# Performance work log

Measured on AMD Instinct MI355X. Metric: run time of the kernel, lower is better.

## Reference

```python
import jax, jax.numpy as jnp
import numpy as np

C_IN, LAT, OUT, EMB = 3, 64, 512, 5
B, H = 128, 128
KS = [4, 4, 3, 4, 2]                       # per-layer dynamic kernel sizes
CHANS = [C_IN, LAT, LAT * 2, LAT * 4, LAT * 8]  # in-channels of each dyn conv
MIX = [(C_IN, LAT), (LAT, LAT * 2), (LAT * 2, LAT * 4), (LAT * 4, LAT * 8), (LAT * 8, OUT)]


def setup_inputs() -> dict:
    key = jax.random.key(0)
    ks = jax.random.split(key, 40)
    nrm = lambda k, shape, s=0.02: jax.random.normal(k, shape, jnp.float32) * s
    inp = {}
    inp["input"] = jax.random.normal(ks[0], (B, C_IN, H, H), jnp.float32)
    inp["label"] = jax.random.randint(ks[1], (B,), 0, 10)
    inp["emb"] = nrm(ks[2], (10, EMB), 1.0)  # label embedding table
    i = 3
    for j, (c, k) in enumerate(zip(CHANS, KS), 1):  # label -> dyn kernel linears
        inp[f"l{j}_w"] = nrm(ks[i], (EMB, c * k * k), 0.1)
        inp[f"l{j}_b"] = jnp.zeros((c * k * k,), jnp.float32)
        i += 1
    for j, (ci, co) in enumerate(MIX, 1):  # channel-mixer linears
        inp[f"cm{j}_w"] = nrm(ks[i], (ci, co))
        inp[f"cm{j}_b"] = jnp.zeros((co,), jnp.float32)
        i += 1
    for j, c in enumerate([LAT, LAT * 2, LAT * 4, LAT * 8], 1):  # BN affine params
        inp[f"bn{j}_g"] = jnp.ones((c,), jnp.float32)
        inp[f"bn{j}_b"] = jnp.zeros((c,), jnp.float32)
    return inp


def dw_conv(x, k, stride, pad):
    """Per-sample, per-channel (depthwise) 2d cross-correlation.
    x: (B,C,H,W), k: (B,C,h,w) -> (B,C,H',W')."""
    def one(xi, ki):
        return jax.lax.conv_general_dilated(
            xi[None], ki[:, None], (stride, stride),
            [(pad, pad), (pad, pad)],
            dimension_numbers=("NCHW", "OIHW", "NCHW"),
            feature_group_count=xi.shape[0])[0]
    return jax.vmap(one)(x, k)


def reference(input, label, emb,
              l1_w, l1_b, l2_w, l2_b, l3_w, l3_b, l4_w, l4_b, l5_w, l5_b,
              cm1_w, cm1_b, cm2_w, cm2_b, cm3_w, cm3_b, cm4_w, cm4_b, cm5_w, cm5_b,
              bn1_g, bn1_b, bn2_g, bn2_b, bn3_g, bn3_b, bn4_g, bn4_b):
    e = emb[label]  # (B, EMB)
    dk = lambda w, b, c, k: jnp.tanh(e @ w + b).reshape(-1, c, k, k)
    k1 = dk(l1_w, l1_b, C_IN, 4)
    k2 = dk(l2_w, l2_b, LAT, 4)
    k3 = dk(l3_w, l3_b, LAT * 2, 3)
    k4 = dk(l4_w, l4_b, LAT * 4, 4)
    k5 = dk(l5_w, l5_b, LAT * 8, 2)

    mix = lambda z, w, b: jnp.einsum("bchw,cd->bdhw", z, w) + b[None, :, None, None]
    lrelu = lambda z: jax.nn.leaky_relu(z, 0.2)

    def bn(z, g, b):  # training-mode BN (batch statistics, biased var, eps=1e-5)
        m = z.mean((0, 2, 3), keepdims=True)
        v = z.var((0, 2, 3), keepdims=True)
        return (z - m) * jax.lax.rsqrt(v + 1e-5) * g[None, :, None, None] + b[None, :, None, None]

    z = bn(lrelu(mix(dw_conv(input, k1, 2, 1), cm1_w, cm1_b)), bn1_g, bn1_b)
    z = bn(lrelu(mix(dw_conv(z, k2, 2, 1), cm2_w, cm2_b)), bn2_g, bn2_b)
    z = bn(lrelu(mix(dw_conv(z, k3, 2, 1), cm3_w, cm3_b)), bn3_g, bn3_b)
    z = bn(lrelu(mix(dw_conv(z, k4, 2, 1), cm4_w, cm4_b)), bn4_g, bn4_b)
    z = jax.nn.sigmoid(mix(dw_conv(z, k5, 1, 0), cm5_w, cm5_b))  # (B, OUT, 7, 7)
    return (z, label)
```

## Files before the change

kernel.cpp:

```cpp
#include <hip/hip_runtime.h>
#include <hip/hip_bf16.h>

typedef __hip_bfloat16 bf16;
using short8  = __attribute__((ext_vector_type(8))) short;
using floatx4 = __attribute__((ext_vector_type(4))) float;

__device__ __forceinline__ float b2f(unsigned short u) {
    union { unsigned int i; float f; } v; v.i = ((unsigned int)u) << 16; return v.f;
}
__device__ __forceinline__ unsigned short f2b(float f) {
    bf16 h = __float2bfloat16(f);
    return *(unsigned short*)&h;
}

#define NREP 16

__global__ __launch_bounds__(256) void prep_kernel(
    const int* __restrict__ label, const float* __restrict__ emb,
    const float* __restrict__ l1w, const float* __restrict__ l1b,
    const float* __restrict__ l2w, const float* __restrict__ l2b,
    const float* __restrict__ l3w, const float* __restrict__ l3b,
    const float* __restrict__ l4w, const float* __restrict__ l4b,
    const float* __restrict__ l5w, const float* __restrict__ l5b,
    float* __restrict__ dynk, float* __restrict__ stats,
    float* __restrict__ labelOut)
{
    const int tid = threadIdx.x;
    if (blockIdx.x == gridDim.x - 1) {
        for (int i = tid; i < 30720; i += 256) stats[i] = 0.0f;
        if (tid < 128) labelOut[tid] = (float)label[tid];
        return;
    }
    int idx = blockIdx.x * 256 + tid;
    if (idx >= 1071104) return;
    const float* w; const float* bb; int loc, ckk;
    if (idx < 6144)        { w = l1w; bb = l1b; loc = idx;          ckk = 48;   }
    else if (idx < 137216) { w = l2w; bb = l2b; loc = idx - 6144;   ckk = 1024; }
    else if (idx < 284672) { w = l3w; bb = l3b; loc = idx - 137216; ckk = 1152; }
    else if (idx < 808960) { w = l4w; bb = l4b; loc = idx - 284672; ckk = 4096; }
    else                   { w = l5w; bb = l5b; loc = idx - 808960; ckk = 2048; }
    int b   = loc / ckk;
    int col = loc - b * ckk;
    int lab = label[b];
    float acc = bb[col];
    #pragma unroll
    for (int m = 0; m < 5; ++m)
        acc = fmaf(emb[lab * 5 + m], w[m * ckk + col], acc);
    dynk[idx] = tanhf(acc);
}

__global__ __launch_bounds__(256) void wt_kernel(
    const float* __restrict__ w2, const float* __restrict__ w3,
    const float* __restrict__ w4, const float* __restrict__ w5,
    bf16* __restrict__ wt2, bf16* __restrict__ wt3,
    bf16* __restrict__ wt4, bf16* __restrict__ wt5)
{
    __shared__ float T[32][33];
    const int tid = threadIdx.x;
    int t = blockIdx.x;
    const float* W; bf16* WT; int K, N, tl;
    if (t < 8)        { W = w2; WT = wt2; K = 64;  N = 128; tl = t; }
    else if (t < 40)  { W = w3; WT = wt3; K = 128; N = 256; tl = t - 8; }
    else if (t < 168) { W = w4; WT = wt4; K = 256; N = 512; tl = t - 40; }
    else              { W = w5; WT = wt5; K = 512; N = 512; tl = t - 168; }
    const int NT = N >> 5;
    const int kt = tl / NT, nt = tl - kt * NT;
    const int k0 = kt * 32, n0 = nt * 32;
    const int cc = tid & 31, rr = tid >> 5;
    #pragma unroll
    for (int it = 0; it < 4; ++it) {
        int k = rr + it * 8;
        T[k][cc] = W[(long)(k0 + k) * N + n0 + cc];
    }
    __syncthreads();
    #pragma unroll
    for (int it = 0; it < 4; ++it) {
        int n = rr + it * 8;
        WT[(long)(n0 + n) * K + k0 + cc] = __float2bfloat16(T[cc][n]);
    }
}

__global__ __launch_bounds__(128) void fused_l1_v3(
    const float* __restrict__ xf, const float* __restrict__ dynk,
    const float* __restrict__ W, const float* __restrict__ bias,
    bf16* __restrict__ y, float* __restrict__ statsOut)
{
    constexpr int HIN = 128, HOUT = 64;
    constexpr int TW = 16, TH = 8;
    constexpr int PS  = 36;
    constexpr int PCH = 18 * PS;

    __shared__ float patch[3 * PCH];
    __shared__ __align__(16) float dwT[16 * 28];
    __shared__ float Wlds[192];
    __shared__ float klds[48];
    __shared__ float biasL[64];
    __shared__ float sums[64], sqs[64];

    const int tid = threadIdx.x;
    const int b   = blockIdx.x >> 5;
    const int tl  = blockIdx.x & 31;
    const int ty0 = (tl >> 2) * TH;
    const int tx0 = (tl & 3) * TW;

    if (tid < 48) klds[tid] = dynk[b * 48 + tid];
    for (int i = tid; i < 192; i += 128) Wlds[i] = W[i];
    if (tid < 64) { biasL[tid] = bias[tid]; sums[tid] = 0.f; sqs[tid] = 0.f; }

    {
        const int iy0 = ty0 * 2 - 1, ix0 = tx0 * 2 - 1;
        for (int i = tid; i < 3 * 18 * 34; i += 128) {
            int c  = i / 612;
            int r  = i - c * 612;
            int py = r / 34, px = r - py * 34;
            int gy = iy0 + py, gx = ix0 + px;
            float v = 0.f;
            if ((unsigned)gy < (unsigned)HIN && (unsigned)gx < (unsigned)HIN)
                v = xf[((long)b * 3 + c) * (HIN * HIN) + gy * HIN + gx];
            patch[c * PCH + py * PS + px] = v;
        }
    }
    __syncthreads();

    {
        const int py = tid >> 4, px = tid & 15;
        const int pixg = tid >> 3, j = tid & 7;
        #pragma unroll
        for (int c = 0; c < 3; ++c) {
            const float* pb = &patch[c * PCH + (py * 2) * PS + px * 2];
            float a = 0.f;
            #pragma unroll
            for (int kh = 0; kh < 4; ++kh)
                #pragma unroll
                for (int kw = 0; kw < 4; ++kw)
                    a = fmaf(pb[kh * PS + kw], klds[c * 16 + kh * 4 + kw], a);
            dwT[pixg * 28 + j * 3 + c] = a;
        }
    }
    __syncthreads();

    {
        const int cq = tid & 7, pixg = tid >> 3;
        const int d0 = cq * 8;
        float Wr[3][8], bi[8];
        #pragma unroll
        for (int c = 0; c < 3; ++c)
            #pragma unroll
            for (int t = 0; t < 8; ++t) Wr[c][t] = Wlds[c * 64 + d0 + t];
        #pragma unroll
        for (int t = 0; t < 8; ++t) bi[t] = biasL[d0 + t];

        float dv[24];
        #pragma unroll
        for (int q4 = 0; q4 < 6; ++q4)
            *(float4*)&dv[q4 * 4] = *(const float4*)&dwT[pixg * 28 + q4 * 4];

        float sreg[8] = {}, qreg[8] = {};
        #pragma unroll
        for (int j = 0; j < 8; ++j) {
            const int pos = pixg * 8 + j;
            const float dv0 = dv[j * 3 + 0];
            const float dv1 = dv[j * 3 + 1];
            const float dv2 = dv[j * 3 + 2];
            const int py = pos >> 4, px = pos & 15;
            const long row = ((long)(b * HOUT + ty0 + py)) * HOUT + tx0 + px;
            union { uint4 v; unsigned short us[8]; } pk;
            #pragma unroll
            for (int t = 0; t < 8; ++t) {
                float v = fmaf(dv0, Wr[0][t], fmaf(dv1, Wr[1][t], fmaf(dv2, Wr[2][t], bi[t])));
                v = v > 0.f ? v : 0.2f * v;
                sreg[t] += v;
                qreg[t] = fmaf(v, v, qreg[t]);
                pk.us[t] = f2b(v);
            }
            *(uint4*)&y[row * 64 + d0] = pk.v;
        }
        #pragma unroll
        for (int m = 8; m < 64; m <<= 1)
            #pragma unroll
            for (int t = 0; t < 8; ++t) {
                sreg[t] += __shfl_xor(sreg[t], m);
                qreg[t] += __shfl_xor(qreg[t], m);
            }
        if ((tid & 63) < 8) {
            #pragma unroll
            for (int t = 0; t < 8; ++t) {
                atomicAdd(&sums[d0 + t], sreg[t]);
                atomicAdd(&sqs [d0 + t], qreg[t]);
            }
        }
    }
    __syncthreads();
    {
        const int rep = blockIdx.x & (NREP - 1);
        if (tid < 64) {
            atomicAdd(&statsOut[rep * 128 + tid],      sums[tid]);
            atomicAdd(&statsOut[rep * 128 + 64 + tid], sqs[tid]);
        }
    }
}

template<int C, int KS, int HIN, int HOUT, int STRIDE, int PAD, int NTHR>
__global__ __launch_bounds__(NTHR) void dw_direct(
    const bf16* __restrict__ x, const float* __restrict__ st,
    const float* __restrict__ gam, const float* __restrict__ bet,
    const float* __restrict__ dynk, bf16* __restrict__ outA, float NINV)
{
    constexpr int G   = C / 8;
    constexpr int KSK = KS * KS;
    static_assert(NTHR == HOUT * G, "one output row per block");

    __shared__ float wlds[KSK * C];
    __shared__ float ksumL[C];
    __shared__ float scaleL[C], shiftL[C];

    const int tid = threadIdx.x;
    const int b   = blockIdx.x / HOUT;
    const int oy  = blockIdx.x % HOUT;

    for (int i = tid; i < KSK * C; i += NTHR) {
        int c = i % C, t = i / C;
        wlds[t * C + c] = dynk[((long)b * C + c) * KSK + t];
    }
    for (int c = tid; c < C; c += NTHR) {
        float s = 0.f, q = 0.f;
        #pragma unroll
        for (int r = 0; r < NREP; ++r) {
            s += st[r * 2 * C + c];
            q += st[r * 2 * C + C + c];
        }
        float m   = s * NINV;
        float var = fmaf(q, NINV, -m * m);
        float scv = gam[c] * rsqrtf(var + 1e-5f);
        scaleL[c] = scv;
        shiftL[c] = fmaf(-m, scv, bet[c]);
    }
    __syncthreads();
    for (int c = tid; c < C; c += NTHR) {
        float s = 0.f;
        #pragma unroll
        for (int t = 0; t < KSK; ++t) s += wlds[t * C + c];
        ksumL[c] = s;
    }
    __syncthreads();

    const int g  = tid % G;
    const int ox = tid / G;
    const int c0 = g * 8;
    const int iy0 = oy * STRIDE - PAD;
    const int ix0 = ox * STRIDE - PAD;

    float acc[8];
    #pragma unroll
    for (int ch = 0; ch < 8; ++ch) acc[ch] = 0.f;

    const bool interior = (iy0 >= 0) && (iy0 + KS <= HIN) &&
                          (ix0 >= 0) && (ix0 + KS <= HIN);
    float r[8];

    if (interior) {
        const bf16* bp = x + ((long)(b * HIN + iy0) * HIN + ix0) * C + c0;
        uint4 v[KSK];
        #pragma unroll
        for (int kh = 0; kh < KS; ++kh)
            #pragma unroll
            for (int kw = 0; kw < KS; ++kw)
                v[kh * KS + kw] = *(const uint4*)(bp + (kh * HIN + kw) * C);
        #pragma unroll
        for (int t = 0; t < KSK; ++t) {
            const float* wp = &wlds[t * C + c0];
            float4 wa = *(const float4*)wp;
            float4 wb = *(const float4*)(wp + 4);
            const float wt[8] = {wa.x, wa.y, wa.z, wa.w, wb.x, wb.y, wb.z, wb.w};
            #pragma unroll
            for (int ch = 0; ch < 8; ++ch) {
                unsigned u = ((const unsigned*)&v[t])[ch >> 1];
                unsigned bits = (ch & 1) ? (u & 0xffff0000u) : (u << 16);
                acc[ch] = fmaf(__uint_as_float(bits), wt[ch], acc[ch]);
            }
        }
        #pragma unroll
        for (int ch = 0; ch < 8; ++ch) {
            float sc = scaleL[c0 + ch], sh = shiftL[c0 + ch], ks = ksumL[c0 + ch];
            r[ch] = fmaf(sc, acc[ch], sh * ks);
        }
    } else {
        float sc[8], sh[8];
        #pragma unroll
        for (int ch = 0; ch < 8; ++ch) { sc[ch] = scaleL[c0 + ch]; sh[ch] = shiftL[c0 + ch]; }
        #pragma unroll
        for (int kh = 0; kh < KS; ++kh) {
            const int iy = iy0 + kh;
            if ((unsigned)iy >= (unsigned)HIN) continue;
            #pragma unroll
            for (int kw = 0; kw < KS; ++kw) {
                const int ix = ix0 + kw;
                if ((unsigned)ix >= (unsigned)HIN) continue;
                uint4 v = *(const uint4*)&x[((long)(b * HIN + iy) * HIN + ix) * C + c0];
                const float* wp = &wlds[(kh * KS + kw) * C + c0];
                float4 wa = *(const float4*)wp;
                float4 wb = *(const float4*)(wp + 4);
                const float wt[8] = {wa.x, wa.y, wa.z, wa.w, wb.x, wb.y, wb.z, wb.w};
                #pragma unroll
                for (int ch = 0; ch < 8; ++ch) {
                    unsigned u = ((const unsigned*)&v)[ch >> 1];
                    unsigned bits = (ch & 1) ? (u & 0xffff0000u) : (u << 16);
                    float xb = fmaf(__uint_as_float(bits), sc[ch], sh[ch]);
                    acc[ch] = fmaf(xb, wt[ch], acc[ch]);
                }
            }
        }
        #pragma unroll
        for (int ch = 0; ch < 8; ++ch) r[ch] = acc[ch];
    }

    union { uint4 v; unsigned short us[8]; } pk;
    #pragma unroll
    for (int ch = 0; ch < 8; ++ch) pk.us[ch] = f2b(r[ch]);
    *(uint4*)&outA[((long)(b * HOUT + oy) * HOUT + ox) * C + c0] = pk.v;
}

template<int K, int COUT, bool LAST>
__global__ __launch_bounds__(256) void gemm_layer(
    const bf16* __restrict__ A, const bf16* __restrict__ WT,
    const float* __restrict__ bias, bf16* __restrict__ y,
    float* __restrict__ statsOut, float* __restrict__ outF, int Mtiles)
{
    constexpr int SK = 72;
    constexpr int CS = 136;
    __shared__ __align__(16) unsigned short smem[18432];
    unsigned short* As  = smem;
    unsigned short* Bs  = smem + 9216;
    unsigned short* Csh = smem;
    __shared__ float sums[128], sqs[128];

    const int tid  = threadIdx.x;
    const int lane = tid & 63;
    const int w    = tid >> 6;
    const int wm   = (w >> 1) * 64, wn = (w & 1) * 64;
    const int lm   = lane & 15, lq = lane >> 4;
    const int mt   = blockIdx.x % Mtiles;
    const int nt   = blockIdx.x / Mtiles;
    const long m0  = (long)mt * 128;
    const int  n0  = nt * 128;

    floatx4 acc[4][4];
    #pragma unroll
    for (int i = 0; i < 4; ++i)
        #pragma unroll
        for (int j = 0; j < 4; ++j) acc[i][j] = (floatx4)0.0f;

    for (int kb = 0; kb < K; kb += 64) {
        __syncthreads();
        #pragma unroll
        for (int s = 0; s < 4; ++s) {
            int i = tid + s * 256;
            int m = i >> 3, q = i & 7;
            uint4 va = *(const uint4*)(A  + ((m0 + m) * K + kb + q * 8));
            uint4 vb = *(const uint4*)(WT + ((long)(n0 + m) * K + kb + q * 8));
            *(uint4*)&As[m * SK + q * 8] = va;
            *(uint4*)&Bs[m * SK + q * 8] = vb;
        }
        __syncthreads();
        #pragma unroll
        for (int h = 0; h < 2; ++h) {
            short8 af[4], bfr[4];
            #pragma unroll
            for (int i = 0; i < 4; ++i) {
                af[i]  = *(const short8*)&As[(wm + i * 16 + lm) * SK + h * 32 + lq * 8];
                bfr[i] = *(const short8*)&Bs[(wn + i * 16 + lm) * SK + h * 32 + lq * 8];
            }
            #pragma unroll
            for (int i = 0; i < 4; ++i)
                #pragma unroll
                for (int j = 0; j < 4; ++j)
                    acc[i][j] = __builtin_amdgcn_mfma_f32_16x16x32_bf16(af[i], bfr[j], acc[i][j], 0, 0, 0);
        }
    }
    __syncthreads();

    float bj[4];
    #pragma unroll
    for (int j = 0; j < 4; ++j) bj[j] = bias[n0 + wn + j * 16 + lm];

    if constexpr (!LAST) {
        if (tid < 128) { sums[tid] = 0.f; sqs[tid] = 0.f; }
        #pragma unroll
        for (int i = 0; i < 4; ++i)
            #pragma unroll
            for (int j = 0; j < 4; ++j) {
                int c = wn + j * 16 + lm;
                #pragma unroll
                for (int rg = 0; rg < 4; ++rg) {
                    int r = wm + i * 16 + lq * 4 + rg;
                    float v = acc[i][j][rg] + bj[j];
                    v = v > 0.f ? v : 0.2f * v;
                    Csh[r * CS + c] = f2b(v);
                }
            }
        __syncthreads();
        const int cg = tid & 15, mr = tid >> 4;
        float sacc[8], qacc[8];
        #pragma unroll
        for (int t = 0; t < 8; ++t) { sacc[t] = 0.f; qacc[t] = 0.f; }
        #pragma unroll
        for (int it = 0; it < 8; ++it) {
            int m = mr + it * 16;
            uint4 pk = *(const uint4*)&Csh[m * CS + cg * 8];
            *(uint4*)&y[(m0 + m) * COUT + n0 + cg * 8] = pk;
            const unsigned short* pu = (const unsigned short*)&pk;
            #pragma unroll
            for (int t = 0; t < 8; ++t) {
                float f = b2f(pu[t]);
                sacc[t] += f;
                qacc[t] = fmaf(f, f, qacc[t]);
            }
        }
        #pragma unroll
        for (int t = 0; t < 8; ++t) {
            atomicAdd(&sums[cg * 8 + t], sacc[t]);
            atomicAdd(&sqs [cg * 8 + t], qacc[t]);
        }
        __syncthreads();
        {
            const int rep = blockIdx.x & (NREP - 1);
            if (tid < 128) {
                atomicAdd(&statsOut[rep * 2 * COUT + n0 + tid],        sums[tid]);
                atomicAdd(&statsOut[rep * 2 * COUT + COUT + n0 + tid], sqs[tid]);
            }
        }
    } else {
        #pragma unroll
        for (int i = 0; i < 4; ++i)
            #pragma unroll
            for (int j = 0; j < 4; ++j) {
                int c  = wn + j * 16 + lm;
                int rb = wm + i * 16 + lq * 4;
                ushort4 pk;
                unsigned short* pp = (unsigned short*)&pk;
                #pragma unroll
                for (int rg = 0; rg < 4; ++rg)
                    pp[rg] = f2b(acc[i][j][rg] + bj[j]);
                *(ushort4*)&Csh[c * CS + rb] = pk;
            }
        __syncthreads();
        const int mg = tid & 15, nr = tid >> 4;
        #pragma unroll
        for (int it = 0; it < 8; ++it) {
            int n = nr + it * 16;
            uint4 pk = *(const uint4*)&Csh[n * CS + mg * 8];
            const unsigned short* pu = (const unsigned short*)&pk;
            #pragma unroll
            for (int t = 0; t < 8; ++t) {
                int m = (int)m0 + mg * 8 + t;
                int b = m / 49, pos = m - b * 49;
                float v = b2f(pu[t]);
                outF[((long)(b * 512 + n0 + n)) * 49 + pos] = 1.f / (1.f + __expf(-v));
            }
        }
    }
}


extern "C" void kernel_launch(void* const* d_in, const int* in_sizes, int n_in,
                              void* d_out, int out_size, void* d_ws, size_t ws_size,
                              hipStream_t stream)
{
    const float* input = (const float*)d_in[0];
    const int*   label = (const int*)d_in[1];
    const float* emb   = (const float*)d_in[2];
    const float* lw[5] = {(const float*)d_in[3], (const float*)d_in[5], (const float*)d_in[7],
                          (const float*)d_in[9], (const float*)d_in[11]};
    const float* lb[5] = {(const float*)d_in[4], (const float*)d_in[6], (const float*)d_in[8],
                          (const float*)d_in[10], (const float*)d_in[12]};
    const float* cmw[5] = {(const float*)d_in[13], (const float*)d_in[15], (const float*)d_in[17],
                           (const float*)d_in[19], (const float*)d_in[21]};
    const float* cmb[5] = {(const float*)d_in[14], (const float*)d_in[16], (const float*)d_in[18],
                           (const float*)d_in[20], (const float*)d_in[22]};
    const float* bng[4] = {(const float*)d_in[23], (const float*)d_in[25],
                           (const float*)d_in[27], (const float*)d_in[29]};
    const float* bnb[4] = {(const float*)d_in[24], (const float*)d_in[26],
                           (const float*)d_in[28], (const float*)d_in[30]};
    float* out = (float*)d_out;

    float* wsf   = (float*)d_ws;
    float* dynk  = wsf;
    float* stats = wsf + 1071104;
    const float* k1 = dynk;
    const float* k2 = dynk + 6144;
    const float* k3 = dynk + 137216;
    const float* k4 = dynk + 284672;
    const float* k5 = dynk + 808960;
    float* st1 = stats;
    float* st2 = stats + 2048;
    float* st3 = stats + 6144;
    float* st4 = stats + 14336;

    bf16* wt  = (bf16*)((char*)d_ws + 4407296);
    bf16* wt2 = wt;
    bf16* wt3 = wt + 8192;
    bf16* wt4 = wt + 40960;
    bf16* wt5 = wt + 172032;
    bf16* S1  = (bf16*)((char*)d_ws + 5308416);
    bf16* S2  = (bf16*)((char*)d_ws + 72417280);

    prep_kernel<<<4186, 256, 0, stream>>>(label, emb,
        lw[0], lb[0], lw[1], lb[1], lw[2], lb[2], lw[3], lb[3], lw[4], lb[4],
        dynk, stats, out + 3211264);
    wt_kernel<<<424, 256, 0, stream>>>(cmw[1], cmw[2], cmw[3], cmw[4],
                                       wt2, wt3, wt4, wt5);

    fused_l1_v3<<<4096, 128, 0, stream>>>(input, k1, cmw[0], cmb[0], S1, st1);

    dw_direct<64, 4, 64, 32, 2, 1, 256><<<4096, 256, 0, stream>>>(
        S1, st1, bng[0], bnb[0], k2, S2, 1.f / 524288.f);
    gemm_layer<64, 128, false><<<1024, 256, 0, stream>>>(
        S2, wt2, cmb[1], S1, st2, nullptr, 1024);

    dw_direct<128, 3, 32, 16, 2, 1, 256><<<2048, 256, 0, stream>>>(
        S1, st2, bng[1], bnb[1], k3, S2, 1.f / 131072.f);
    gemm_layer<128, 256, false><<<512, 256, 0, stream>>>(
        S2, wt3, cmb[2], S1, st3, nullptr, 256);

    dw_direct<256, 4, 16, 8, 2, 1, 256><<<1024, 256, 0, stream>>>(
        S1, st3, bng[2], bnb[2], k4, S2, 1.f / 32768.f);
    gemm_layer<256, 512, false><<<256, 256, 0, stream>>>(
        S2, wt4, cmb[3], S1, st4, nullptr, 64);

    dw_direct<512, 2, 8, 7, 1, 0, 448><<<896, 448, 0, stream>>>(
        S1, st4, bng[3], bnb[3], k5, S2, 1.f / 8192.f);
    gemm_layer<512, 512, true><<<196, 256, 0, stream>>>(
        S2, wt5, cmb[4], nullptr, nullptr, out, 49);
}
```

Measured before the change: 347.8 us.

## Pretranspose dynamic kernels and hoist BN affine prep out of depthwise conv

The prep kernel now writes the dynamic depthwise kernels in a tap-major (t, c) layout, so each dw_direct block copies its weights to shared memory with contiguous float4 loads instead of a strided gather. BN scale and shift are computed once per layer by a small bn_prep kernel rather than redundantly in every block. The interior path applies the affine to each input before the multiply, which removes the ksum precompute and one barrier. The cost is four extra kernel launches and more FMAs per tap in the inner loop.

```diff
diff --git a/kernel.cpp b/kernel.cpp
--- a/kernel.cpp
+++ b/kernel.cpp
@@ -33,12 +33,12 @@
     }
     int idx = blockIdx.x * 256 + tid;
     if (idx >= 1071104) return;
-    const float* w; const float* bb; int loc, ckk;
-    if (idx < 6144)        { w = l1w; bb = l1b; loc = idx;          ckk = 48;   }
-    else if (idx < 137216) { w = l2w; bb = l2b; loc = idx - 6144;   ckk = 1024; }
-    else if (idx < 284672) { w = l3w; bb = l3b; loc = idx - 137216; ckk = 1152; }
-    else if (idx < 808960) { w = l4w; bb = l4b; loc = idx - 284672; ckk = 4096; }
-    else                   { w = l5w; bb = l5b; loc = idx - 808960; ckk = 2048; }
+    const float* w; const float* bb; int loc, ckk, ksk, base;
+    if (idx < 6144)        { w = l1w; bb = l1b; loc = idx;          ckk = 48;   ksk = 0;  base = 0;      }
+    else if (idx < 137216) { w = l2w; bb = l2b; loc = idx - 6144;   ckk = 1024; ksk = 16; base = 6144;   }
+    else if (idx < 284672) { w = l3w; bb = l3b; loc = idx - 137216; ckk = 1152; ksk = 9;  base = 137216; }
+    else if (idx < 808960) { w = l4w; bb = l4b; loc = idx - 284672; ckk = 4096; ksk = 16; base = 284672; }
+    else                   { w = l5w; bb = l5b; loc = idx - 808960; ckk = 2048; ksk = 4;  base = 808960; }
     int b   = loc / ckk;
     int col = loc - b * ckk;
     int lab = label[b];
@@ -46,7 +46,34 @@
     #pragma unroll
     for (int m = 0; m < 5; ++m)
         acc = fmaf(emb[lab * 5 + m], w[m * ckk + col], acc);
-    dynk[idx] = tanhf(acc);
+    float val = tanhf(acc);
+    if (ksk == 0) {
+        dynk[idx] = val;
+    } else {
+        int c  = col / ksk;
+        int t  = col - c * ksk;
+        int Cl = ckk / ksk;
+        dynk[base + b * ckk + t * Cl + c] = val;
+    }
+}
+
+__global__ void bn_prep(const float* __restrict__ st,
+                        const float* __restrict__ gam, const float* __restrict__ bet,
+                        float* __restrict__ aff, int C, float NINV)
+{
+    int c = threadIdx.x;
+    if (c >= C) return;
+    float s = 0.f, q = 0.f;
+    #pragma unroll
+    for (int r = 0; r < NREP; ++r) {
+        s += st[r * 2 * C + c];
+        q += st[r * 2 * C + C + c];
+    }
+    float m   = s * NINV;
+    float var = fmaf(q, NINV, -m * m);
+    float sc  = gam[c] * rsqrtf(var + 1e-5f);
+    aff[c]     = sc;
+    aff[C + c] = fmaf(-m, sc, bet[c]);
 }
 
 __global__ __launch_bounds__(256) void wt_kernel(
@@ -202,45 +229,23 @@
 
 template<int C, int KS, int HIN, int HOUT, int STRIDE, int PAD, int NTHR>
 __global__ __launch_bounds__(NTHR) void dw_direct(
-    const bf16* __restrict__ x, const float* __restrict__ st,
-    const float* __restrict__ gam, const float* __restrict__ bet,
-    const float* __restrict__ dynk, bf16* __restrict__ outA, float NINV)
+    const bf16* __restrict__ x, const float* __restrict__ aff,
+    const float* __restrict__ dynkT, bf16* __restrict__ outA)
 {
     constexpr int G   = C / 8;
     constexpr int KSK = KS * KS;
     static_assert(NTHR == HOUT * G, "one output row per block");
 
-    __shared__ float wlds[KSK * C];
-    __shared__ float ksumL[C];
-    __shared__ float scaleL[C], shiftL[C];
+    __shared__ __align__(16) float wlds[KSK * C];
 
     const int tid = threadIdx.x;
     const int b   = blockIdx.x / HOUT;
     const int oy  = blockIdx.x % HOUT;
 
-    for (int i = tid; i < KSK * C; i += NTHR) {
-        int c = i % C, t = i / C;
-        wlds[t * C + c] = dynk[((long)b * C + c) * KSK + t];
-    }
-    for (int c = tid; c < C; c += NTHR) {
-        float s = 0.f, q = 0.f;
-        #pragma unroll
-        for (int r = 0; r < NREP; ++r) {
-            s += st[r * 2 * C + c];
-            q += st[r * 2 * C + C + c];
-        }
-        float m   = s * NINV;
-        float var = fmaf(q, NINV, -m * m);
-        float scv = gam[c] * rsqrtf(var + 1e-5f);
-        scaleL[c] = scv;
-        shiftL[c] = fmaf(-m, scv, bet[c]);
-    }
-    __syncthreads();
-    for (int c = tid; c < C; c += NTHR) {
-        float s = 0.f;
-        #pragma unroll
-        for (int t = 0; t < KSK; ++t) s += wlds[t * C + c];
-        ksumL[c] = s;
+    {
+        const float* src = dynkT + (long)b * (KSK * C);
+        for (int i = tid * 4; i < KSK * C; i += NTHR * 4)
+            *(float4*)&wlds[i] = *(const float4*)&src[i];
     }
     __syncthreads();
 
@@ -250,13 +255,24 @@
     const int iy0 = oy * STRIDE - PAD;
     const int ix0 = ox * STRIDE - PAD;
 
+    float sc[8], sh[8];
+    {
+        float4 a0 = *(const float4*)&aff[c0];
+        float4 a1 = *(const float4*)&aff[c0 + 4];
+        float4 b0 = *(const float4*)&aff[C + c0];
+        float4 b1 = *(const float4*)&aff[C + c0 + 4];
+        sc[0]=a0.x; sc[1]=a0.y; sc[2]=a0.z; sc[3]=a0.w;
+        sc[4]=a1.x; sc[5]=a1.y; sc[6]=a1.z; sc[7]=a1.w;
+        sh[0]=b0.x; sh[1]=b0.y; sh[2]=b0.z; sh[3]=b0.w;
+        sh[4]=b1.x; sh[5]=b1.y; sh[6]=b1.z; sh[7]=b1.w;
+    }
+
     float acc[8];
     #pragma unroll
     for (int ch = 0; ch < 8; ++ch) acc[ch] = 0.f;
 
     const bool interior = (iy0 >= 0) && (iy0 + KS <= HIN) &&
                           (ix0 >= 0) && (ix0 + KS <= HIN);
-    float r[8];
 
     if (interior) {
         const bf16* bp = x + ((long)(b * HIN + iy0) * HIN + ix0) * C + c0;
@@ -276,18 +292,11 @@
             for (int ch = 0; ch < 8; ++ch) {
                 unsigned u = ((const unsigned*)&v[t])[ch >> 1];
                 unsigned bits = (ch & 1) ? (u & 0xffff0000u) : (u << 16);
-                acc[ch] = fmaf(__uint_as_float(bits), wt[ch], acc[ch]);
-            }
-        }
-        #pragma unroll
-        for (int ch = 0; ch < 8; ++ch) {
-            float sc = scaleL[c0 + ch], sh = shiftL[c0 + ch], ks = ksumL[c0 + ch];
-            r[ch] = fmaf(sc, acc[ch], sh * ks);
+                float xb = fmaf(__uint_as_float(bits), sc[ch], sh[ch]);
+                acc[ch] = fmaf(xb, wt[ch], acc[ch]);
+            }
         }
     } else {
-        float sc[8], sh[8];
-        #pragma unroll
-        for (int ch = 0; ch < 8; ++ch) { sc[ch] = scaleL[c0 + ch]; sh[ch] = shiftL[c0 + ch]; }
         #pragma unroll
         for (int kh = 0; kh < KS; ++kh) {
             const int iy = iy0 + kh;
@@ -310,13 +319,11 @@
                 }
             }
         }
-        #pragma unroll
-        for (int ch = 0; ch < 8; ++ch) r[ch] = acc[ch];
     }
 
     union { uint4 v; unsigned short us[8]; } pk;
     #pragma unroll
-    for (int ch = 0; ch < 8; ++ch) pk.us[ch] = f2b(r[ch]);
+    for (int ch = 0; ch < 8; ++ch) pk.us[ch] = f2b(acc[ch]);
     *(uint4*)&outA[((long)(b * HOUT + oy) * HOUT + ox) * C + c0] = pk.v;
 }
 
@@ -486,11 +493,11 @@
     float* wsf   = (float*)d_ws;
     float* dynk  = wsf;
     float* stats = wsf + 1071104;
-    const float* k1 = dynk;
-    const float* k2 = dynk + 6144;
-    const float* k3 = dynk + 137216;
-    const float* k4 = dynk + 284672;
-    const float* k5 = dynk + 808960;
+    const float* k1  = dynk;
+    const float* k2T = dynk + 6144;
+    const float* k3T = dynk + 137216;
+    const float* k4T = dynk + 284672;
+    const float* k5T = dynk + 808960;
     float* st1 = stats;
     float* st2 = stats + 2048;
     float* st3 = stats + 6144;
@@ -503,6 +510,11 @@
     bf16* wt5 = wt + 172032;
     bf16* S1  = (bf16*)((char*)d_ws + 5308416);
     bf16* S2  = (bf16*)((char*)d_ws + 72417280);
+    float* affBase = (float*)((char*)d_ws + 89194496);
+    float* aff1 = affBase;
+    float* aff2 = affBase + 128;
+    float* aff3 = affBase + 384;
+    float* aff4 = affBase + 896;
 
     prep_kernel<<<4186, 256, 0, stream>>>(label, emb,
         lw[0], lb[0], lw[1], lb[1], lw[2], lb[2], lw[3], lb[3], lw[4], lb[4],
@@ -512,23 +524,23 @@
 
     fused_l1_v3<<<4096, 128, 0, stream>>>(input, k1, cmw[0], cmb[0], S1, st1);
 
-    dw_direct<64, 4, 64, 32, 2, 1, 256><<<4096, 256, 0, stream>>>(
-        S1, st1, bng[0], bnb[0], k2, S2, 1.f / 524288.f);
+    bn_prep<<<1, 64, 0, stream>>>(st1, bng[0], bnb[0], aff1, 64, 1.f / 524288.f);
+    dw_direct<64, 4, 64, 32, 2, 1, 256><<<4096, 256, 0, stream>>>(S1, aff1, k2T, S2);
     gemm_layer<64, 128, false><<<1024, 256, 0, stream>>>(
         S2, wt2, cmb[1], S1, st2, nullptr, 1024);
 
-    dw_direct<128, 3, 32, 16, 2, 1, 256><<<2048, 256, 0, stream>>>(
-        S1, st2, bng[1], bnb[1], k3, S2, 1.f / 131072.f);
+    bn_prep<<<1, 128, 0, stream>>>(st2, bng[1], bnb[1], aff2, 128, 1.f / 131072.f);
+    dw_direct<128, 3, 32, 16, 2, 1, 256><<<2048, 256, 0, stream>>>(S1, aff2, k3T, S2);
     gemm_layer<128, 256, false><<<512, 256, 0, stream>>>(
         S2, wt3, cmb[2], S1, st3, nullptr, 256);
 
-    dw_direct<256, 4, 16, 8, 2, 1, 256><<<1024, 256, 0, stream>>>(
-        S1, st3, bng[2], bnb[2], k4, S2, 1.f / 32768.f);
+    bn_prep<<<1, 256, 0, stream>>>(st3, bng[2], bnb[2], aff3, 256, 1.f / 32768.f);
+    dw_direct<256, 4, 16, 8, 2, 1, 256><<<1024, 256, 0, stream>>>(S1, aff3, k4T, S2);
     gemm_layer<256, 512, false><<<256, 256, 0, stream>>>(
         S2, wt4, cmb[3], S1, st4, nullptr, 64);
 
-    dw_direct<512, 2, 8, 7, 1, 0, 448><<<896, 448, 0, stream>>>(
-        S1, st4, bng[3], bnb[3], k5, S2, 1.f / 8192.f);
+    bn_prep<<<1, 512, 0, stream>>>(st4, bng[3], bnb[3], aff4, 512, 1.f / 8192.f);
+    dw_direct<512, 2, 8, 7, 1, 0, 448><<<896, 448, 0, stream>>>(S1, aff4, k5T, S2);
     gemm_layer<512, 512, true><<<196, 256, 0, stream>>>(
         S2, wt5, cmb[4], nullptr, nullptr, out, 49);
 }
```

Measured after the change: 328.3 us. -5.6%, faster.
